# Performance work log

Hardware: AMD Instinct MI355X
Metric: run time of the kernel (lower is better)

The kernel has to match this reference:

```python
import jax, jax.numpy as jnp
import numpy as np

KERNEL_SIZE = 3
DILATION = 1


def setup_inputs() -> dict:
    key = jax.random.key(0)
    k1, k2, k3 = jax.random.split(key, 3)
    B, C, T = 8, 512, 4096
    OUT = 512
    x = jax.random.normal(k1, (B, C, T), dtype=jnp.float32)
    # nn.Linear weight: (out_features, in_features=C*kernel_size)
    W = jax.random.normal(k2, (OUT, C * KERNEL_SIZE), dtype=jnp.float32) * 0.02
    b = jax.random.normal(k3, (OUT,), dtype=jnp.float32) * 0.02
    return {"x": x, "W": W, "b": b}


def reference(x, W, b):
    # UnfoldConv1d forward: causal unfold (im2col) -> transpose -> linear -> transpose.
    # TemporalUnfold1d left-pads with (k-1)*dilation zeros, unfolds with kernel k,
    # then gathers rows so the feature axis is ordered (kernel_pos, channel):
    # row j*C + c at time t equals x[b, c, t - (k-1-j)*dilation] (zero-padded).
    K, D = KERNEL_SIZE, DILATION
    B, C, T = x.shape
    pad = (K - 1) * D
    xp = jnp.pad(x, ((0, 0), (0, 0), (pad, 0)))  # (B, C, T+pad)
    # unf[b, j, c, t] = xp[b, c, t + j*D] ; j=K-1 corresponds to current timestep
    unf = jnp.stack([xp[:, :, j * D: j * D + T] for j in range(K)], axis=1)  # (B, K, C, T)
    unf = unf.reshape(B, K * C, T)
    # transpose(1,2) -> linear -> transpose(1,2) == einsum over feature axis
    y = jnp.einsum('bft,of->bot', unf, W) + b[None, :, None]  # (B, OUT, T)
    return y
```

## Files before the change

### kernel.cpp

```cpp
#include <hip/hip_runtime.h>
#include <stdint.h>


typedef float    f32x4  __attribute__((ext_vector_type(4)));
typedef short    bf16x8 __attribute__((ext_vector_type(8)));

#define C_DIM   512
#define T_DIM   4096
#define TP_DIM  4104
#define OUT_DIM 512
#define KF_DIM  1536
#define B_DIM   8

__device__ __forceinline__ uint16_t f2bf(float f) {
  union { float f; uint32_t u; } v; v.f = f;
  uint32_t u = v.u;
  return (uint16_t)((u + 0x7fffu + ((u >> 16) & 1u)) >> 16);
}

__device__ __forceinline__ void gload_lds16(const uint16_t* g, uint16_t* l) {
  __builtin_amdgcn_global_load_lds(
      (const __attribute__((address_space(1))) uint32_t*)g,
      (__attribute__((address_space(3))) uint32_t*)l, 16, 0, 0);
}

__global__ __launch_bounds__(256) void prep_w(const float* __restrict__ W,
                                              uint16_t* __restrict__ Wb) {
  int i = blockIdx.x * 256 + threadIdx.x;
  if (i >= 196608) return;
  float4 v = ((const float4*)W)[i];
  ushort4 o;
  o.x = f2bf(v.x); o.y = f2bf(v.y); o.z = f2bf(v.z); o.w = f2bf(v.w);
  ((ushort4*)Wb)[i] = o;
}

__global__ __launch_bounds__(256) void prep_x(const float* __restrict__ x,
                                              uint16_t* __restrict__ xp) {
  __shared__ uint16_t tile[128 * 65];
  const int tid = threadIdx.x;
  const int tp0 = blockIdx.x * 64;
  const int c0  = blockIdx.y * 128;
  const int b   = blockIdx.z;

  const int p = tid & 31;
  const int t = tp0 - 2 + p * 2;
  const bool ok = (t >= 0) && (t < T_DIM);
  #pragma unroll
  for (int it = 0; it < 16; ++it) {
    int cr = it * 8 + (tid >> 5);
    float vx = 0.f, vy = 0.f;
    if (ok) {
      const float2 v = *(const float2*)(x + (long)(b * C_DIM + c0 + cr) * T_DIM + t);
      vx = v.x; vy = v.y;
    }
    tile[cr * 65 + 2 * p]     = f2bf(vx);
    tile[cr * 65 + 2 * p + 1] = f2bf(vy);
  }
  __syncthreads();

  const int q = tid & 31;
  #pragma unroll
  for (int it = 0; it < 8; ++it) {
    int r = it * 8 + (tid >> 5);
    int tp = tp0 + r;
    if (tp < TP_DIM) {
      ushort4 val;
      val.x = tile[(4 * q + 0) * 65 + r];
      val.y = tile[(4 * q + 1) * 65 + r];
      val.z = tile[(4 * q + 2) * 65 + r];
      val.w = tile[(4 * q + 3) * 65 + r];
      *(ushort4*)(xp + (long)(b * TP_DIM + tp) * C_DIM + c0 + 4 * q) = val;
    }
  }
}

__global__ __launch_bounds__(256) void gemm_kernel(const uint16_t* __restrict__ xp,
                                                   const uint16_t* __restrict__ Wb,
                                                   const float* __restrict__ bias,
                                                   float* __restrict__ out) {
  __shared__ uint16_t XT[136 * 64];
  __shared__ uint16_t WS[128 * 64];

  const int tid  = threadIdx.x;
  const int lane = tid & 63;
  const int wid  = tid >> 6;
  const int wm   = wid >> 1;
  const int wn   = wid & 1;
  const int t0 = blockIdx.x * 128;
  const int o0 = blockIdx.y * 128;
  const int b  = blockIdx.z;

  f32x4 acc[4][4];
  #pragma unroll
  for (int mi = 0; mi < 4; ++mi)
    #pragma unroll
    for (int ni = 0; ni < 4; ++ni)
      #pragma unroll
      for (int r = 0; r < 4; ++r) acc[mi][ni][r] = 0.0f;

  const uint16_t* xbase = xp + ((long)b * TP_DIM + t0) * C_DIM;
  const int g = lane >> 4;

  for (int c0 = 0; c0 < C_DIM; c0 += 64) {
    #pragma unroll
    for (int j = 0; j < 3; ++j) {
      __syncthreads();
      if (j == 0) {
        #pragma unroll
        for (int it = 0; it < 4; ++it) {
          int u = it * 256 + tid;
          int row = u >> 3, ch = u & 7;
          const uint16_t* src = xbase + (long)row * C_DIM + c0 + ((ch ^ (row & 7)) << 3);
          gload_lds16(src, &XT[(it * 256 + wid * 64) * 8]);
        }
        if (tid < 64) {
          int u = 1024 + tid;
          int row = u >> 3, ch = u & 7;
          const uint16_t* src = xbase + (long)row * C_DIM + c0 + ((ch ^ (row & 7)) << 3);
          gload_lds16(src, &XT[1024 * 8]);
        }
      }
      {
        const uint16_t* wbase = Wb + (long)o0 * KF_DIM + j * C_DIM + c0;
        #pragma unroll
        for (int it = 0; it < 4; ++it) {
          int u = it * 256 + tid;
          int row = u >> 3, ch = u & 7;
          const uint16_t* src = wbase + (long)row * KF_DIM + ((ch ^ (row & 7)) << 3);
          gload_lds16(src, &WS[(it * 256 + wid * 64) * 8]);
        }
      }
      __syncthreads();

      #pragma unroll
      for (int cc = 0; cc < 2; ++cc) {
        bf16x8 af[4], bfr[4];
        #pragma unroll
        for (int mi = 0; mi < 4; ++mi) {
          int row = wm * 64 + mi * 16 + (lane & 15);
          int chs = (cc * 4 + g) ^ (row & 7);
          af[mi] = *(const bf16x8*)&WS[row * 64 + chs * 8];
        }
        #pragma unroll
        for (int ni = 0; ni < 4; ++ni) {
          int row = wn * 64 + ni * 16 + (lane & 15) + j;
          int chs = (cc * 4 + g) ^ (row & 7);
          bfr[ni] = *(const bf16x8*)&XT[row * 64 + chs * 8];
        }
        #pragma unroll
        for (int mi = 0; mi < 4; ++mi)
          #pragma unroll
          for (int ni = 0; ni < 4; ++ni)
            acc[mi][ni] = __builtin_amdgcn_mfma_f32_16x16x32_bf16(
                af[mi], bfr[ni], acc[mi][ni], 0, 0, 0);
      }
    }
  }

  #pragma unroll
  for (int mi = 0; mi < 4; ++mi) {
    int orow = o0 + wm * 64 + mi * 16 + (lane >> 4) * 4;
    #pragma unroll
    for (int ni = 0; ni < 4; ++ni) {
      int t = t0 + wn * 64 + ni * 16 + (lane & 15);
      float* op = out + ((long)b * OUT_DIM + orow) * T_DIM + t;
      #pragma unroll
      for (int r = 0; r < 4; ++r)
        op[(long)r * T_DIM] = acc[mi][ni][r] + bias[orow + r];
    }
  }
}

__global__ __launch_bounds__(256) void naive_kernel(const float* __restrict__ x,
                                                    const float* __restrict__ W,
                                                    const float* __restrict__ bias,
                                                    float* __restrict__ y) {
  int t = blockIdx.x * 256 + threadIdx.x;
  int o = blockIdx.y, b = blockIdx.z;
  float s = bias[o];
  #pragma unroll
  for (int j = 0; j < 3; ++j) {
    int tt = t - 2 + j;
    if (tt < 0) continue;
    const float* xr = x + (long)b * C_DIM * T_DIM + tt;
    const float* wr = W + (long)o * KF_DIM + j * C_DIM;
    float a = 0.f;
    for (int c = 0; c < C_DIM; ++c) a += wr[c] * xr[(long)c * T_DIM];
    s += a;
  }
  y[((long)b * OUT_DIM + o) * T_DIM + t] = s;
}

extern "C" void kernel_launch(void* const* d_in, const int* in_sizes, int n_in,
                              void* d_out, int out_size, void* d_ws, size_t ws_size,
                              hipStream_t stream) {
  (void)in_sizes; (void)n_in; (void)out_size;
  const float* x    = (const float*)d_in[0];
  const float* W    = (const float*)d_in[1];
  const float* bias = (const float*)d_in[2];
  float* out = (float*)d_out;

  const size_t wb_elems = (size_t)OUT_DIM * KF_DIM;
  const size_t xp_elems = (size_t)B_DIM * TP_DIM * C_DIM;
  const size_t need = (wb_elems + xp_elems) * sizeof(uint16_t);

  if (ws_size < need) {
    naive_kernel<<<dim3(T_DIM / 256, OUT_DIM, B_DIM), 256, 0, stream>>>(x, W, bias, out);
    return;
  }

  uint16_t* Wb = (uint16_t*)d_ws;
  uint16_t* xp = (uint16_t*)d_ws + wb_elems;

  prep_w<<<768, 256, 0, stream>>>(W, Wb);
  prep_x<<<dim3(65, 4, 8), 256, 0, stream>>>(x, xp);
  gemm_kernel<<<dim3(32, 4, 8), 256, 0, stream>>>(xp, Wb, bias, out);
}
```

Measured before the change: 83.27 us.

## Rewrite GEMM with 256x256 tiles and a double-buffered, prioritized LDS pipeline

Replaces the 128x128, 256-thread GEMM with a 256x256-tile, 512-thread kernel. It double-buffers A and B tiles in LDS and stages the next k-tiles with async global-to-LDS loads, interleaved between MFMA quarter-blocks. Explicit waitcnt and barriers plus s_setprio are used so loads overlap with matrix math, and the larger tile raises arithmetic intensity. In exchange, the shifted X rows are no longer reused across kernel taps, so each tap's B tile is reloaded. LDS use (128KB) and register pressure also limit the GPU to one block per CU, and the grid is now exactly 256 blocks.

```diff
diff --git a/kernel.cpp b/kernel.cpp
--- a/kernel.cpp
+++ b/kernel.cpp
@@ -22,6 +22,150 @@
   __builtin_amdgcn_global_load_lds(
       (const __attribute__((address_space(1))) uint32_t*)g,
       (__attribute__((address_space(3))) uint32_t*)l, 16, 0, 0);
+}
+
+__device__ __forceinline__ void stage_a(const uint16_t* __restrict__ a,
+                                        uint16_t* lds, int r0, int tid) {
+  int row = r0 + (tid >> 3);
+  const uint16_t* src = a + (long)row * KF_DIM + (((tid & 7) ^ (row & 7)) << 3);
+  gload_lds16(src, lds + r0 * 64 + (tid >> 6) * 512);
+}
+
+__device__ __forceinline__ void stage_b(const uint16_t* __restrict__ bt,
+                                        uint16_t* lds, int r0, int tid) {
+  int L = r0 + (tid >> 3);
+  int n = ((L >> 5) & 3) * 64 + (L >> 7) * 32 + (L & 31);
+  const uint16_t* src = bt + (long)n * C_DIM + (((tid & 7) ^ (L & 7)) << 3);
+  gload_lds16(src, lds + r0 * 64 + (tid >> 6) * 512);
+}
+
+#define BAR()   __builtin_amdgcn_s_barrier()
+#define LGKM0() asm volatile("s_waitcnt lgkmcnt(0)" ::: "memory")
+#define LGKM8() asm volatile("s_waitcnt lgkmcnt(8)" ::: "memory")
+#define VM(n)   asm volatile("s_waitcnt vmcnt(" #n ")" ::: "memory")
+#define PRIO1() __builtin_amdgcn_s_setprio(1)
+#define PRIO0() __builtin_amdgcn_s_setprio(0)
+
+#define READ_A(BUF, MH) do { \
+  _Pragma("unroll") for (int mi = 0; mi < 4; ++mi) { \
+    const int row_ = wm * 128 + (MH) * 64 + mi * 16 + lr; \
+    _Pragma("unroll") for (int kk = 0; kk < 2; ++kk) \
+      af[mi][kk] = *(const bf16x8*)&(BUF)[row_ * 64 + (((kk * 4 + g) ^ (lr & 7)) << 3)]; \
+  } } while (0)
+
+#define READ_B(BUF, NH) do { \
+  _Pragma("unroll") for (int ni = 0; ni < 2; ++ni) { \
+    const int row_ = (NH) * 128 + wn * 32 + ni * 16 + lr; \
+    _Pragma("unroll") for (int kk = 0; kk < 2; ++kk) \
+      bfrag[ni][kk] = *(const bf16x8*)&(BUF)[row_ * 64 + (((kk * 4 + g) ^ (lr & 7)) << 3)]; \
+  } } while (0)
+
+#define MFMA16(MH, NH) do { PRIO1(); \
+  _Pragma("unroll") for (int mi = 0; mi < 4; ++mi) \
+  _Pragma("unroll") for (int ni = 0; ni < 2; ++ni) \
+  _Pragma("unroll") for (int kk = 0; kk < 2; ++kk) \
+    acc[(MH) * 4 + mi][(NH) * 2 + ni] = __builtin_amdgcn_mfma_f32_16x16x32_bf16( \
+        af[mi][kk], bfrag[ni][kk], acc[(MH) * 4 + mi][(NH) * 2 + ni], 0, 0, 0); \
+  PRIO0(); } while (0)
+
+__device__ __forceinline__ const uint16_t* btile(const uint16_t* xsrc, int kb) {
+  return xsrc + (kb >> 3) * C_DIM + ((kb & 7) << 6);
+}
+
+template<int MODE>
+__device__ __forceinline__ void ktile(
+    f32x4 (&acc)[8][4], bf16x8 (&af)[4][2], bf16x8 (&bfrag)[2][2],
+    uint16_t* cA, uint16_t* cB, uint16_t* oA, uint16_t* oB,
+    const uint16_t* __restrict__ wsrc, const uint16_t* __restrict__ xsrc,
+    int kt, int tid, int wm, int wn, int lr, int g) {
+  const uint16_t* aN1 = wsrc + (kt + 1) * 64;
+  const uint16_t* bN1 = btile(xsrc, kt + 1);
+  const uint16_t* aN2 = wsrc + (kt + 2) * 64;
+  const uint16_t* bN2 = btile(xsrc, kt + 2);
+
+  READ_A(cA, 0); READ_B(cB, 0);
+  if (MODE <= 1) { stage_b(bN1, oB, 0, tid); stage_b(bN1, oB, 64, tid); }
+  LGKM8();
+  BAR(); LGKM0(); MFMA16(0, 0); BAR();
+  READ_B(cB, 1);
+  if (MODE <= 1) { stage_a(aN1, oA, 128, tid); stage_a(aN1, oA, 192, tid); }
+  BAR(); LGKM0(); MFMA16(0, 1); BAR();
+  READ_A(cA, 1);
+  if (MODE == 0) { stage_a(aN2, cA, 0, tid); stage_a(aN2, cA, 64, tid); }
+  BAR(); LGKM0(); MFMA16(1, 1); BAR();
+  READ_B(cB, 0);
+  if (MODE == 0) { stage_b(bN2, cB, 128, tid); stage_b(bN2, cB, 192, tid); }
+  BAR(); LGKM0(); MFMA16(1, 0);
+  if (MODE == 0) { VM(4); }
+  else if (MODE == 1) { VM(0); }
+  BAR();
+}
+
+__global__ __launch_bounds__(512, 2) void gemm_kernel(
+    const uint16_t* __restrict__ xp, const uint16_t* __restrict__ Wb,
+    const float* __restrict__ bias, float* __restrict__ out) {
+  __shared__ __align__(16) uint16_t LA0[256 * 64];
+  __shared__ __align__(16) uint16_t LB0[256 * 64];
+  __shared__ __align__(16) uint16_t LA1[256 * 64];
+  __shared__ __align__(16) uint16_t LB1[256 * 64];
+
+  const int tid  = threadIdx.x;
+  const int lane = tid & 63;
+  const int wid  = tid >> 6;
+  const int wm   = wid >> 2;
+  const int wn   = wid & 3;
+  const int lr   = lane & 15;
+  const int g    = lane >> 4;
+  const int t0 = blockIdx.x * 256;
+  const int o0 = blockIdx.y * 256;
+  const int b  = blockIdx.z;
+
+  const uint16_t* wsrc = Wb + (long)o0 * KF_DIM;
+  const uint16_t* xsrc = xp + ((long)b * TP_DIM + t0) * C_DIM;
+
+  f32x4 acc[8][4];
+  #pragma unroll
+  for (int mi = 0; mi < 8; ++mi)
+    #pragma unroll
+    for (int ni = 0; ni < 4; ++ni)
+      #pragma unroll
+      for (int r = 0; r < 4; ++r) acc[mi][ni][r] = 0.0f;
+
+  bf16x8 af[4][2], bfrag[2][2];
+
+  {
+    const uint16_t* a1 = wsrc + 64;
+    const uint16_t* b1 = btile(xsrc, 1);
+    stage_a(wsrc, LA0, 0, tid);   stage_a(wsrc, LA0, 64, tid);
+    stage_a(wsrc, LA0, 128, tid); stage_a(wsrc, LA0, 192, tid);
+    stage_b(xsrc, LB0, 0, tid);   stage_b(xsrc, LB0, 64, tid);
+    stage_b(xsrc, LB0, 128, tid); stage_b(xsrc, LB0, 192, tid);
+    stage_a(a1, LA1, 0, tid);     stage_a(a1, LA1, 64, tid);
+    stage_b(b1, LB1, 128, tid);   stage_b(b1, LB1, 192, tid);
+    VM(4);
+    BAR();
+  }
+
+  #pragma unroll 1
+  for (int i = 0; i < 11; ++i) {
+    ktile<0>(acc, af, bfrag, LA0, LB0, LA1, LB1, wsrc, xsrc, 2 * i,     tid, wm, wn, lr, g);
+    ktile<0>(acc, af, bfrag, LA1, LB1, LA0, LB0, wsrc, xsrc, 2 * i + 1, tid, wm, wn, lr, g);
+  }
+  ktile<1>(acc, af, bfrag, LA0, LB0, LA1, LB1, wsrc, xsrc, 22, tid, wm, wn, lr, g);
+  ktile<2>(acc, af, bfrag, LA1, LB1, LA0, LB0, wsrc, xsrc, 23, tid, wm, wn, lr, g);
+
+  #pragma unroll
+  for (int mi = 0; mi < 8; ++mi) {
+    int orow = o0 + wm * 128 + mi * 16 + (lane >> 4) * 4;
+    #pragma unroll
+    for (int ni = 0; ni < 4; ++ni) {
+      int t = t0 + wn * 64 + ni * 16 + lr;
+      float* op = out + ((long)b * OUT_DIM + orow) * T_DIM + t;
+      #pragma unroll
+      for (int r = 0; r < 4; ++r)
+        op[(long)r * T_DIM] = acc[mi][ni][r] + bias[orow + r];
+    }
+  }
 }
 
 __global__ __launch_bounds__(256) void prep_w(const float* __restrict__ W,
@@ -74,103 +218,6 @@
   }
 }
 
-__global__ __launch_bounds__(256) void gemm_kernel(const uint16_t* __restrict__ xp,
-                                                   const uint16_t* __restrict__ Wb,
-                                                   const float* __restrict__ bias,
-                                                   float* __restrict__ out) {
-  __shared__ uint16_t XT[136 * 64];
-  __shared__ uint16_t WS[128 * 64];
-
-  const int tid  = threadIdx.x;
-  const int lane = tid & 63;
-  const int wid  = tid >> 6;
-  const int wm   = wid >> 1;
-  const int wn   = wid & 1;
-  const int t0 = blockIdx.x * 128;
-  const int o0 = blockIdx.y * 128;
-  const int b  = blockIdx.z;
-
-  f32x4 acc[4][4];
-  #pragma unroll
-  for (int mi = 0; mi < 4; ++mi)
-    #pragma unroll
-    for (int ni = 0; ni < 4; ++ni)
-      #pragma unroll
-      for (int r = 0; r < 4; ++r) acc[mi][ni][r] = 0.0f;
-
-  const uint16_t* xbase = xp + ((long)b * TP_DIM + t0) * C_DIM;
-  const int g = lane >> 4;
-
-  for (int c0 = 0; c0 < C_DIM; c0 += 64) {
-    #pragma unroll
-    for (int j = 0; j < 3; ++j) {
-      __syncthreads();
-      if (j == 0) {
-        #pragma unroll
-        for (int it = 0; it < 4; ++it) {
-          int u = it * 256 + tid;
-          int row = u >> 3, ch = u & 7;
-          const uint16_t* src = xbase + (long)row * C_DIM + c0 + ((ch ^ (row & 7)) << 3);
-          gload_lds16(src, &XT[(it * 256 + wid * 64) * 8]);
-        }
-        if (tid < 64) {
-          int u = 1024 + tid;
-          int row = u >> 3, ch = u & 7;
-          const uint16_t* src = xbase + (long)row * C_DIM + c0 + ((ch ^ (row & 7)) << 3);
-          gload_lds16(src, &XT[1024 * 8]);
-        }
-      }
-      {
-        const uint16_t* wbase = Wb + (long)o0 * KF_DIM + j * C_DIM + c0;
-        #pragma unroll
-        for (int it = 0; it < 4; ++it) {
-          int u = it * 256 + tid;
-          int row = u >> 3, ch = u & 7;
-          const uint16_t* src = wbase + (long)row * KF_DIM + ((ch ^ (row & 7)) << 3);
-          gload_lds16(src, &WS[(it * 256 + wid * 64) * 8]);
-        }
-      }
-      __syncthreads();
-
-      #pragma unroll
-      for (int cc = 0; cc < 2; ++cc) {
-        bf16x8 af[4], bfr[4];
-        #pragma unroll
-        for (int mi = 0; mi < 4; ++mi) {
-          int row = wm * 64 + mi * 16 + (lane & 15);
-          int chs = (cc * 4 + g) ^ (row & 7);
-          af[mi] = *(const bf16x8*)&WS[row * 64 + chs * 8];
-        }
-        #pragma unroll
-        for (int ni = 0; ni < 4; ++ni) {
-          int row = wn * 64 + ni * 16 + (lane & 15) + j;
-          int chs = (cc * 4 + g) ^ (row & 7);
-          bfr[ni] = *(const bf16x8*)&XT[row * 64 + chs * 8];
-        }
-        #pragma unroll
-        for (int mi = 0; mi < 4; ++mi)
-          #pragma unroll
-          for (int ni = 0; ni < 4; ++ni)
-            acc[mi][ni] = __builtin_amdgcn_mfma_f32_16x16x32_bf16(
-                af[mi], bfr[ni], acc[mi][ni], 0, 0, 0);
-      }
-    }
-  }
-
-  #pragma unroll
-  for (int mi = 0; mi < 4; ++mi) {
-    int orow = o0 + wm * 64 + mi * 16 + (lane >> 4) * 4;
-    #pragma unroll
-    for (int ni = 0; ni < 4; ++ni) {
-      int t = t0 + wn * 64 + ni * 16 + (lane & 15);
-      float* op = out + ((long)b * OUT_DIM + orow) * T_DIM + t;
-      #pragma unroll
-      for (int r = 0; r < 4; ++r)
-        op[(long)r * T_DIM] = acc[mi][ni][r] + bias[orow + r];
-    }
-  }
-}
-
 __global__ __launch_bounds__(256) void naive_kernel(const float* __restrict__ x,
                                                     const float* __restrict__ W,
                                                     const float* __restrict__ bias,
@@ -214,5 +261,5 @@
 
   prep_w<<<768, 256, 0, stream>>>(W, Wb);
   prep_x<<<dim3(65, 4, 8), 256, 0, stream>>>(x, xp);
-  gemm_kernel<<<dim3(32, 4, 8), 256, 0, stream>>>(xp, Wb, bias, out);
-}
+  gemm_kernel<<<dim3(16, 2, 8), 512, 0, stream>>>(xp, Wb, bias, out);
+}
```

Result: slower. 88.48 us (+6.3%).

## Fuse weight/input prep kernels, widen GEMM time tile, swap operands for vector stores

Applied to the files above, without the earlier changes.

Merges the weight bf16 conversion into the input transpose/pad kernel as an extra z-slice, removing one launch. The GEMM tile grows from 128 to 256 timesteps per block with 8x4 accumulators per wave, so each weight tile loaded into LDS is reused across twice as many timesteps. MFMA operands are swapped so time becomes the row dimension. This lets each lane store four contiguous timesteps as one 16-byte vector store, and bias is hoisted into registers. The cost is higher register pressure and LDS use, and the grid halves to 512 blocks, which may reduce occupancy.

```diff
diff --git a/kernel.cpp b/kernel.cpp
--- a/kernel.cpp
+++ b/kernel.cpp
@@ -24,20 +24,22 @@
       (__attribute__((address_space(3))) uint32_t*)l, 16, 0, 0);
 }
 
-__global__ __launch_bounds__(256) void prep_w(const float* __restrict__ W,
-                                              uint16_t* __restrict__ Wb) {
-  int i = blockIdx.x * 256 + threadIdx.x;
-  if (i >= 196608) return;
-  float4 v = ((const float4*)W)[i];
-  ushort4 o;
-  o.x = f2bf(v.x); o.y = f2bf(v.y); o.z = f2bf(v.z); o.w = f2bf(v.w);
-  ((ushort4*)Wb)[i] = o;
-}
-
-__global__ __launch_bounds__(256) void prep_x(const float* __restrict__ x,
-                                              uint16_t* __restrict__ xp) {
+__global__ __launch_bounds__(256) void prep_all(const float* __restrict__ x,
+                                                const float* __restrict__ W,
+                                                uint16_t* __restrict__ Wb,
+                                                uint16_t* __restrict__ xp) {
+  const int tid = threadIdx.x;
+  if (blockIdx.z == 8) {
+    int flat = blockIdx.y * 65 + blockIdx.x;
+    for (int i = flat * 256 + tid; i < 196608; i += 260 * 256) {
+      float4 v = ((const float4*)W)[i];
+      ushort4 o;
+      o.x = f2bf(v.x); o.y = f2bf(v.y); o.z = f2bf(v.z); o.w = f2bf(v.w);
+      ((ushort4*)Wb)[i] = o;
+    }
+    return;
+  }
   __shared__ uint16_t tile[128 * 65];
-  const int tid = threadIdx.x;
   const int tp0 = blockIdx.x * 64;
   const int c0  = blockIdx.y * 128;
   const int b   = blockIdx.z;
@@ -78,7 +80,7 @@
                                                    const uint16_t* __restrict__ Wb,
                                                    const float* __restrict__ bias,
                                                    float* __restrict__ out) {
-  __shared__ uint16_t XT[136 * 64];
+  __shared__ uint16_t XT[264 * 64];
   __shared__ uint16_t WS[128 * 64];
 
   const int tid  = threadIdx.x;
@@ -86,20 +88,26 @@
   const int wid  = tid >> 6;
   const int wm   = wid >> 1;
   const int wn   = wid & 1;
-  const int t0 = blockIdx.x * 128;
+  const int lr   = lane & 15;
+  const int g    = lane >> 4;
+  const int t0 = blockIdx.x * 256;
   const int o0 = blockIdx.y * 128;
   const int b  = blockIdx.z;
 
-  f32x4 acc[4][4];
-  #pragma unroll
-  for (int mi = 0; mi < 4; ++mi)
+  const uint16_t* xbase = xp + ((long)b * TP_DIM + t0) * C_DIM;
+
+  f32x4 acc[8][4];
+  #pragma unroll
+  for (int mi = 0; mi < 8; ++mi)
     #pragma unroll
     for (int ni = 0; ni < 4; ++ni)
       #pragma unroll
       for (int r = 0; r < 4; ++r) acc[mi][ni][r] = 0.0f;
 
-  const uint16_t* xbase = xp + ((long)b * TP_DIM + t0) * C_DIM;
-  const int g = lane >> 4;
+  float bias_v[4];
+  #pragma unroll
+  for (int ni = 0; ni < 4; ++ni)
+    bias_v[ni] = bias[o0 + wn * 64 + ni * 16 + lr];
 
   for (int c0 = 0; c0 < C_DIM; c0 += 64) {
     #pragma unroll
@@ -107,17 +115,17 @@
       __syncthreads();
       if (j == 0) {
         #pragma unroll
-        for (int it = 0; it < 4; ++it) {
+        for (int it = 0; it < 8; ++it) {
           int u = it * 256 + tid;
           int row = u >> 3, ch = u & 7;
           const uint16_t* src = xbase + (long)row * C_DIM + c0 + ((ch ^ (row & 7)) << 3);
           gload_lds16(src, &XT[(it * 256 + wid * 64) * 8]);
         }
         if (tid < 64) {
-          int u = 1024 + tid;
+          int u = 2048 + tid;
           int row = u >> 3, ch = u & 7;
           const uint16_t* src = xbase + (long)row * C_DIM + c0 + ((ch ^ (row & 7)) << 3);
-          gload_lds16(src, &XT[1024 * 8]);
+          gload_lds16(src, &XT[2048 * 8]);
         }
       }
       {
@@ -134,39 +142,36 @@
 
       #pragma unroll
       for (int cc = 0; cc < 2; ++cc) {
-        bf16x8 af[4], bfr[4];
-        #pragma unroll
-        for (int mi = 0; mi < 4; ++mi) {
-          int row = wm * 64 + mi * 16 + (lane & 15);
-          int chs = (cc * 4 + g) ^ (row & 7);
-          af[mi] = *(const bf16x8*)&WS[row * 64 + chs * 8];
+        bf16x8 af[8], bf[4];
+        #pragma unroll
+        for (int mi = 0; mi < 8; ++mi) {
+          int row = wm * 128 + mi * 16 + lr + j;
+          af[mi] = *(const bf16x8*)&XT[row * 64 + (((cc * 4 + g) ^ (row & 7)) << 3)];
         }
         #pragma unroll
         for (int ni = 0; ni < 4; ++ni) {
-          int row = wn * 64 + ni * 16 + (lane & 15) + j;
-          int chs = (cc * 4 + g) ^ (row & 7);
-          bfr[ni] = *(const bf16x8*)&XT[row * 64 + chs * 8];
-        }
-        #pragma unroll
-        for (int mi = 0; mi < 4; ++mi)
+          int row = wn * 64 + ni * 16 + lr;
+          bf[ni] = *(const bf16x8*)&WS[row * 64 + (((cc * 4 + g) ^ (lr & 7)) << 3)];
+        }
+        #pragma unroll
+        for (int mi = 0; mi < 8; ++mi)
           #pragma unroll
           for (int ni = 0; ni < 4; ++ni)
             acc[mi][ni] = __builtin_amdgcn_mfma_f32_16x16x32_bf16(
-                af[mi], bfr[ni], acc[mi][ni], 0, 0, 0);
+                af[mi], bf[ni], acc[mi][ni], 0, 0, 0);
       }
     }
   }
 
   #pragma unroll
-  for (int mi = 0; mi < 4; ++mi) {
-    int orow = o0 + wm * 64 + mi * 16 + (lane >> 4) * 4;
+  for (int mi = 0; mi < 8; ++mi) {
+    int tcoord = t0 + wm * 128 + mi * 16 + g * 4;
     #pragma unroll
     for (int ni = 0; ni < 4; ++ni) {
-      int t = t0 + wn * 64 + ni * 16 + (lane & 15);
-      float* op = out + ((long)b * OUT_DIM + orow) * T_DIM + t;
-      #pragma unroll
-      for (int r = 0; r < 4; ++r)
-        op[(long)r * T_DIM] = acc[mi][ni][r] + bias[orow + r];
+      int o = o0 + wn * 64 + ni * 16 + lr;
+      f32x4 v = acc[mi][ni];
+      v[0] += bias_v[ni]; v[1] += bias_v[ni]; v[2] += bias_v[ni]; v[3] += bias_v[ni];
+      *(f32x4*)(out + ((long)b * OUT_DIM + o) * T_DIM + tcoord) = v;
     }
   }
 }
@@ -212,7 +217,6 @@
   uint16_t* Wb = (uint16_t*)d_ws;
   uint16_t* xp = (uint16_t*)d_ws + wb_elems;
 
-  prep_w<<<768, 256, 0, stream>>>(W, Wb);
-  prep_x<<<dim3(65, 4, 8), 256, 0, stream>>>(x, xp);
-  gemm_kernel<<<dim3(32, 4, 8), 256, 0, stream>>>(xp, Wb, bias, out);
-}
+  prep_all<<<dim3(65, 4, 9), 256, 0, stream>>>(x, W, Wb, xp);
+  gemm_kernel<<<dim3(16, 4, 8), 256, 0, stream>>>(xp, Wb, bias, out);
+}
```

Result: slower. 96.78 us (+16.2%).
